# Kernel tuning notes

Hardware: AMD Instinct MI355X
Metric: run time of the kernel (lower is better)

## Reference

```python
import jax, jax.numpy as jnp
import numpy as np

B, S, E, H = 64, 100, 512, 1024  # H must equal 2*E (bmm in attention)
VS, VT, P = 32000, 32000, 100


def setup_inputs() -> dict:
    key = jax.random.key(0)
    ks = jax.random.split(key, 16)
    sc = 0.02
    return {
        "source_sentences": jax.random.randint(ks[0], (B, S), 0, VS),
        "positions": jax.random.randint(ks[1], (B, S), 0, P),
        "target_words": jax.random.randint(ks[2], (B,), 0, VT),
        "source_lengths": jnp.full((B,), S, dtype=jnp.int64 if jax.config.jax_enable_x64 else jnp.int32),
        "max_len": S,
        "emb_in": jax.random.normal(ks[3], (VS, E), jnp.float32) * sc,
        "emb_out": jax.random.normal(ks[4], (VT, E), jnp.float32) * sc,
        "emb_pos": jax.random.normal(ks[5], (P, E), jnp.float32) * sc,
        "W_scale": jax.random.normal(ks[6], (H, 2 * E), jnp.float32) * sc,
        "b_scale": jnp.zeros((H,), jnp.float32),
        "W_ih": jax.random.normal(ks[7], (H, E + H), jnp.float32) * sc,
        "b_ih": jnp.zeros((H,), jnp.float32),
        "W_hh": jax.random.normal(ks[8], (H, H), jnp.float32) * sc,
        "b_hh": jnp.zeros((H,), jnp.float32),
        "W_proj": jax.random.normal(ks[9], (VT, H), jnp.float32) * sc,
        "b_proj": jnp.zeros((VT,), jnp.float32),
    }


def reference(source_sentences, positions, target_words, source_lengths, max_len,
              emb_in, emb_out, emb_pos, W_scale, b_scale,
              W_ih, b_ih, W_hh, b_hh, W_proj, b_proj):
    # --- encoder_forward ---
    words = emb_in[source_sentences]              # [B,S,E]
    pos = emb_pos[positions]                      # [B,S,E]
    enc = jnp.concatenate([words, pos], axis=-1)  # [B,S,2E] combined embeddings
    h0 = jnp.mean(enc, axis=1) @ W_scale.T + b_scale  # [B,H]
    # --- attention (vectorized form of the per-position bmm loop) ---
    energy = jnp.einsum('bh,bsh->bs', h0, enc)        # [B,S]
    align = jax.nn.softmax(energy, axis=1)            # softmax over source positions
    # original uses torch.mean (not sum) over positions
    context = jnp.mean(align[:, :, None] * enc, axis=1)  # [B,2E] == [B,H]
    # --- decoder step ---
    out_w = emb_out[target_words]                      # [B,E]
    x = jnp.concatenate([out_w, context], axis=-1)     # [B,E+H]
    # nn.RNN single step, tanh nonlinearity
    h = jnp.tanh(x @ W_ih.T + b_ih + h0 @ W_hh.T + b_hh)  # [B,H]
    out = h @ W_proj.T + b_proj                        # [B,VT]
    return (out, h)
```

## Files before the change

kernel.cpp:

```cpp
#include <hip/hip_runtime.h>

typedef __attribute__((ext_vector_type(8))) __bf16 bf16x8;
typedef __attribute__((ext_vector_type(4))) float  f32x4;
typedef unsigned short u16;

__device__ __forceinline__ u16 f2bf(float f) {
    union { float f; unsigned int i; } v; v.f = f;
    unsigned int r = v.i + 0x7fffu + ((v.i >> 16) & 1u);
    return (u16)(r >> 16);
}
__device__ __forceinline__ unsigned pack2(float a, float b) {
    union { float f; unsigned u; } x, y; x.f = a; y.f = b;
    return __builtin_amdgcn_perm(y.u + 0x8000u, x.u + 0x8000u, 0x07060302u);
}

#define B_  64
#define S_  100
#define E_  512
#define H_  1024
#define VT_ 32000
#define Kc  128
#define PITCH 128
#define NS2 4
#define NS4 10


__global__ __launch_bounds__(256, 1)
void k1_encmean(const int* __restrict__ src, const int* __restrict__ pos,
                const float* __restrict__ emb_in, const float* __restrict__ emb_pos,
                u16* __restrict__ encmean) {
    int b = blockIdx.x, q4 = blockIdx.y, t = threadIdx.x;
    __shared__ int sidx[S_], pidx[S_];
    __shared__ float part[256][4];
    if (t < S_) { sidx[t] = src[b * S_ + t]; pidx[t] = pos[b * S_ + t]; }
    __syncthreads();

    int f4 = t & 63, g = t >> 6;
    bool isPos = (q4 >= 2);
    const float* base = isPos ? emb_pos : emb_in;
    const int*   idx  = isPos ? pidx : sidx;
    int col = (q4 & 1) * 256 + f4 * 4;

    float a0 = 0.f, a1 = 0.f, a2 = 0.f, a3 = 0.f;
    int s0 = g * 25;
    #pragma unroll
    for (int s = s0; s < s0 + 25; s++) {
        const float4 v = *(const float4*)(base + (size_t)idx[s] * E_ + col);
        a0 += v.x; a1 += v.y; a2 += v.z; a3 += v.w;
    }
    part[t][0] = a0; part[t][1] = a1; part[t][2] = a2; part[t][3] = a3;
    __syncthreads();

    if (t < 64) {
        const float inv = 1.0f / (float)S_;
        float r0 = 0.f, r1 = 0.f, r2 = 0.f, r3 = 0.f;
        #pragma unroll
        for (int g2 = 0; g2 < 4; g2++) {
            r0 += part[g2 * 64 + t][0]; r1 += part[g2 * 64 + t][1];
            r2 += part[g2 * 64 + t][2]; r3 += part[g2 * 64 + t][3];
        }
        int e = q4 * 256 + t * 4;
        u16* o = encmean + (size_t)b * (2 * E_) + e;
        o[0] = f2bf(r0 * inv); o[1] = f2bf(r1 * inv);
        o[2] = f2bf(r2 * inv); o[3] = f2bf(r3 * inv);
    }
}

#define MFMA16(a, bfrag, c) __builtin_amdgcn_mfma_f32_16x16x32_bf16((a), (bfrag), (c), 0, 0, 0)

template<int KLEN, int LDA, int LDW>
__device__ __forceinline__ void gemm_lds(const u16* __restrict__ A,
                                         const float* __restrict__ W,
                                         int jt, int koff, u16* __restrict__ ldsW,
                                         f32x4 acc[4], int t) {
    constexpr int NC = KLEN / Kc;
    const int lane = t & 63, w = t >> 6, m = lane & 15, q = lane >> 4;
    const int r = t >> 2, c4 = t & 3;
    const float* wsrc = W + (size_t)(jt + r) * LDW + koff + c4 * 4;
    const u16*   arow = A + (size_t)(w * 16 + m) * LDA + koff + q * 8;
    const int halfoff = (c4 & 1) * 4;

    float4 v[8];
    #pragma unroll
    for (int i = 0; i < 8; i++) v[i] = *(const float4*)(wsrc + i * 16);
    #pragma unroll
    for (int i = 0; i < 8; i++) {
        int U = (c4 >> 1) + 2 * i;
        uint2 p; p.x = pack2(v[i].x, v[i].y); p.y = pack2(v[i].z, v[i].w);
        *(uint2*)(ldsW + r * PITCH + ((U ^ (r & 15)) * 8) + halfoff) = p;
    }
    __syncthreads();

    for (int c = 0; c < NC; c++) {
        if (c + 1 < NC) {
            #pragma unroll
            for (int i = 0; i < 8; i++)
                v[i] = *(const float4*)(wsrc + (c + 1) * Kc + i * 16);
        }
        const u16* lb = ldsW + (c & 1) * (64 * PITCH);
        const u16* ar = arow + c * Kc;
        #pragma unroll
        for (int ks = 0; ks < 4; ks++) {
            bf16x8 a = *(const bf16x8*)(ar + ks * 32);
            #pragma unroll
            for (int f = 0; f < 4; f++) {
                int rr = f * 16 + m;
                int U  = ks * 4 + q;
                bf16x8 bfr = *(const bf16x8*)(lb + rr * PITCH + ((U ^ (rr & 15)) * 8));
                acc[f] = MFMA16(a, bfr, acc[f]);
            }
        }
        if (c + 1 < NC) {
            u16* wd = ldsW + ((c + 1) & 1) * (64 * PITCH) + r * PITCH;
            #pragma unroll
            for (int i = 0; i < 8; i++) {
                int U = (c4 >> 1) + 2 * i;
                uint2 p; p.x = pack2(v[i].x, v[i].y); p.y = pack2(v[i].z, v[i].w);
                *(uint2*)(wd + ((U ^ (r & 15)) * 8) + halfoff) = p;
            }
        }
        __syncthreads();
    }
}

__global__ __launch_bounds__(256, 2)
void k2_h0p(const u16* __restrict__ encmean, const float* __restrict__ Wscale,
            float* __restrict__ part2) {
    __shared__ u16 ldsW[2 * 64 * PITCH];
    int t = threadIdx.x, lane = t & 63, w = t >> 6, m = lane & 15, q = lane >> 4;
    int jt = blockIdx.x * 64, sp = blockIdx.y;
    f32x4 acc[4] = {{0,0,0,0},{0,0,0,0},{0,0,0,0},{0,0,0,0}};
    gemm_lds<256, 2 * E_, 2 * E_>(encmean, Wscale, jt, sp * 256, ldsW, acc, t);
    #pragma unroll
    for (int f = 0; f < 4; f++) {
        int j = jt + 16 * f + m;
        #pragma unroll
        for (int r2 = 0; r2 < 4; r2++) {
            int bb = w * 16 + q * 4 + r2;
            part2[(size_t)(sp * B_ + bb) * H_ + j] = acc[f][r2];
        }
    }
}

__global__ __launch_bounds__(256, 1)
void k3_attn(const int* __restrict__ src, const int* __restrict__ pos,
             const int* __restrict__ tgt,
             const float* __restrict__ emb_in, const float* __restrict__ emb_pos,
             const float* __restrict__ emb_out,
             const float* __restrict__ part2, const float* __restrict__ bscale,
             u16* __restrict__ x, u16* __restrict__ h0b) {
    int b = blockIdx.x, t = threadIdx.x;
    __shared__ float h0s[2 * E_];
    __shared__ int sidx[S_], pidx[S_];
    __shared__ float energy[S_];
    __shared__ float align_s[S_];

    for (int i = t; i < 2 * E_; i += 256) {
        float v = bscale[i];
        #pragma unroll
        for (int ks = 0; ks < NS2; ks++) v += part2[(size_t)(ks * B_ + b) * H_ + i];
        h0s[i] = v;
        h0b[(size_t)b * H_ + i] = f2bf(v);
    }
    if (t < S_) { sidx[t] = src[b * S_ + t]; pidx[t] = pos[b * S_ + t]; }
    __syncthreads();

    int lane = t & 63, w = t >> 6;
    for (int s = w; s < S_; s += 4) {
        const float* ri = emb_in  + (size_t)sidx[s] * E_;
        const float* rp = emb_pos + (size_t)pidx[s] * E_;
        float acc = 0.f;
        #pragma unroll
        for (int ii = 0; ii < 8; ii++) { int k = lane + 64 * ii; acc += ri[k] * h0s[k]; }
        #pragma unroll
        for (int ii = 0; ii < 8; ii++) { int k = lane + 64 * ii; acc += rp[k] * h0s[E_ + k]; }
        #pragma unroll
        for (int off = 32; off; off >>= 1) acc += __shfl_down(acc, off);
        if (lane == 0) energy[s] = acc;
    }
    __syncthreads();

    if (t < 64) {
        float e0 = energy[t];
        float e1 = (t + 64 < S_) ? energy[t + 64] : -1e30f;
        float mx = fmaxf(e0, e1);
        #pragma unroll
        for (int off = 32; off; off >>= 1) mx = fmaxf(mx, __shfl_xor(mx, off));
        float p0 = expf(e0 - mx);
        float p1 = (t + 64 < S_) ? expf(e1 - mx) : 0.f;
        float ss = p0 + p1;
        #pragma unroll
        for (int off = 32; off; off >>= 1) ss += __shfl_xor(ss, off);
        float inv = 1.0f / (ss * (float)S_);
        align_s[t] = p0 * inv;
        if (t + 64 < S_) align_s[t + 64] = p1 * inv;
    }
    __syncthreads();

    if (t < 128) {
        int o = t;
        bool isPos = (o >= 64);
        const float* base = isPos ? emb_pos : emb_in;
        const int* idx  = isPos ? pidx : sidx;
        int eo = (o & 63) * 8;
        float c[8] = {0,0,0,0,0,0,0,0};
        #pragma unroll 4
        for (int s = 0; s < S_; s++) {
            const float* row = base + (size_t)idx[s] * E_ + eo;
            float al = align_s[s];
            const float4 v0 = *(const float4*)(row);
            const float4 v1 = *(const float4*)(row + 4);
            c[0] += al * v0.x; c[1] += al * v0.y; c[2] += al * v0.z; c[3] += al * v0.w;
            c[4] += al * v1.x; c[5] += al * v1.y; c[6] += al * v1.z; c[7] += al * v1.w;
        }
        u16* xo = x + (size_t)b * (E_ + H_) + E_ + o * 8;
        #pragma unroll
        for (int i = 0; i < 8; i++) xo[i] = f2bf(c[i]);
    } else {
        int i = t - 128;
        int tw = tgt[b];
        const float4 v = *((const float4*)(emb_out + (size_t)tw * E_) + i);
        ushort4 o; o.x = f2bf(v.x); o.y = f2bf(v.y); o.z = f2bf(v.z); o.w = f2bf(v.w);
        *((ushort4*)(x + (size_t)b * (E_ + H_)) + i) = o;
    }
}

__global__ __launch_bounds__(256, 2)
void k4_hp(const u16* __restrict__ xb, const float* __restrict__ Wih,
           const u16* __restrict__ h0b, const float* __restrict__ Whh,
           float* __restrict__ part4) {
    __shared__ u16 ldsW[2 * 64 * PITCH];
    int t = threadIdx.x, lane = t & 63, w = t >> 6, m = lane & 15, q = lane >> 4;
    int jt = blockIdx.x * 64, sp = blockIdx.y;
    f32x4 acc[4] = {{0,0,0,0},{0,0,0,0},{0,0,0,0},{0,0,0,0}};
    if (sp < 6) gemm_lds<256, E_ + H_, E_ + H_>(xb,  Wih, jt, sp * 256,       ldsW, acc, t);
    else        gemm_lds<256, H_,      H_     >(h0b, Whh, jt, (sp - 6) * 256, ldsW, acc, t);
    #pragma unroll
    for (int f = 0; f < 4; f++) {
        int j = jt + 16 * f + m;
        #pragma unroll
        for (int r2 = 0; r2 < 4; r2++) {
            int bb = w * 16 + q * 4 + r2;
            part4[(size_t)(sp * B_ + bb) * H_ + j] = acc[f][r2];
        }
    }
}

__global__ __launch_bounds__(256, 1)
void k4_red(const float* __restrict__ part4,
            const float* __restrict__ bih, const float* __restrict__ bhh,
            float* __restrict__ houtf, u16* __restrict__ hbf) {
    int b = blockIdx.x, t = threadIdx.x;
    int j = t * 4;
    float4 s  = *(const float4*)(bih + j);
    const float4 b2 = *(const float4*)(bhh + j);
    s.x += b2.x; s.y += b2.y; s.z += b2.z; s.w += b2.w;
    #pragma unroll
    for (int ks = 0; ks < NS4; ks++) {
        const float4 p = *(const float4*)(part4 + (size_t)(ks * B_ + b) * H_ + j);
        s.x += p.x; s.y += p.y; s.z += p.z; s.w += p.w;
    }
    float4 h; h.x = tanhf(s.x); h.y = tanhf(s.y); h.z = tanhf(s.z); h.w = tanhf(s.w);
    *(float4*)(houtf + (size_t)b * H_ + j) = h;
    ushort4 o; o.x = f2bf(h.x); o.y = f2bf(h.y); o.z = f2bf(h.z); o.w = f2bf(h.w);
    *(ushort4*)(hbf + (size_t)b * H_ + j) = o;
}

__global__ __launch_bounds__(256, 2)
void k5_out(const u16* __restrict__ hb, const float* __restrict__ Wp,
            const float* __restrict__ bp, float* __restrict__ out) {
    __shared__ u16 ldsW[2 * 64 * PITCH];
    int t = threadIdx.x, lane = t & 63, w = t >> 6, m = lane & 15, q = lane >> 4;
    int jt = blockIdx.x * 64;
    f32x4 acc[4] = {{0,0,0,0},{0,0,0,0},{0,0,0,0},{0,0,0,0}};
    gemm_lds<H_, H_, H_>(hb, Wp, jt, 0, ldsW, acc, t);
    #pragma unroll
    for (int f = 0; f < 4; f++) {
        int j = jt + 16 * f + m;
        float bias = bp[j];
        #pragma unroll
        for (int r = 0; r < 4; r++) {
            int b = w * 16 + q * 4 + r;
            out[(size_t)b * VT_ + j] = acc[f][r] + bias;
        }
    }
}

extern "C" void kernel_launch(void* const* d_in, const int* in_sizes, int n_in,
                              void* d_out, int out_size, void* d_ws, size_t ws_size,
                              hipStream_t stream) {
    const int*   src     = (const int*)d_in[0];
    const int*   pos     = (const int*)d_in[1];
    const int*   tgt     = (const int*)d_in[2];
    const float* emb_in  = (const float*)d_in[5];
    const float* emb_out = (const float*)d_in[6];
    const float* emb_pos = (const float*)d_in[7];
    const float* Wscale  = (const float*)d_in[8];
    const float* bscale  = (const float*)d_in[9];
    const float* Wih     = (const float*)d_in[10];
    const float* bih     = (const float*)d_in[11];
    const float* Whh     = (const float*)d_in[12];
    const float* bhh     = (const float*)d_in[13];
    const float* Wproj   = (const float*)d_in[14];
    const float* bproj   = (const float*)d_in[15];

    char* ws = (char*)d_ws;
    u16*   encmean = (u16*)(ws);
    u16*   xb      = (u16*)(ws + 131072);
    u16*   h0b     = (u16*)(ws + 327680);
    u16*   hbf     = (u16*)(ws + 458752);
    float* part2   = (float*)(ws + 589824);
    float* part4   = (float*)(ws + 1638400);

    float* out   = (float*)d_out;
    float* houtf = out + (size_t)B_ * VT_;

    hipLaunchKernelGGL(k1_encmean, dim3(B_, 4),        dim3(256), 0, stream,
                       src, pos, emb_in, emb_pos, encmean);
    hipLaunchKernelGGL(k2_h0p,     dim3(H_ / 64, NS2), dim3(256), 0, stream,
                       encmean, Wscale, part2);
    hipLaunchKernelGGL(k3_attn,    dim3(B_),           dim3(256), 0, stream,
                       src, pos, tgt, emb_in, emb_pos, emb_out, part2, bscale,
                       xb, h0b);
    hipLaunchKernelGGL(k4_hp,      dim3(H_ / 64, NS4), dim3(256), 0, stream,
                       xb, Wih, h0b, Whh, part4);
    hipLaunchKernelGGL(k4_red,     dim3(B_),           dim3(256), 0, stream,
                       part4, bih, bhh, houtf, hbf);
    hipLaunchKernelGGL(k5_out,     dim3(VT_ / 64),     dim3(256), 0, stream,
                       hbf, Wproj, bproj, out);
}
```

Baseline: 319.6 us.

## Replace LDS-staged weight GEMM with direct register-loaded MFMA fragments; split attention context

Drops the LDS double-buffered weight staging in the GEMM helper. Each wave now loads its own fp32 weight rows from global memory, packs them to bf16 and feeds them straight into MFMA, looping over the four batch groups with A read from global. This removes the LDS stores and barriers on the weight-streaming path (the dominant cost is the 32000x1024 projection). The trade-off is less load coalescing and more global reads of the A operand. The attention kernel also splits the context reduction across all 256 threads via shared-memory partials, and launch bounds change for k2/k4.

```diff
diff --git a/kernel.cpp b/kernel.cpp
--- a/kernel.cpp
+++ b/kernel.cpp
@@ -19,8 +19,6 @@
 #define E_  512
 #define H_  1024
 #define VT_ 32000
-#define Kc  128
-#define PITCH 128
 #define NS2 4
 #define NS4 10
 
@@ -68,76 +66,43 @@
 
 #define MFMA16(a, bfrag, c) __builtin_amdgcn_mfma_f32_16x16x32_bf16((a), (bfrag), (c), 0, 0, 0)
 
-template<int KLEN, int LDA, int LDW>
-__device__ __forceinline__ void gemm_lds(const u16* __restrict__ A,
-                                         const float* __restrict__ W,
-                                         int jt, int koff, u16* __restrict__ ldsW,
-                                         f32x4 acc[4], int t) {
-    constexpr int NC = KLEN / Kc;
+template<int NKC, int LDA, int LDW>
+__device__ __forceinline__ void gemm_direct(const u16* __restrict__ A,
+                                            const float* __restrict__ W,
+                                            int jt, int koff, f32x4 acc[4], int t) {
     const int lane = t & 63, w = t >> 6, m = lane & 15, q = lane >> 4;
-    const int r = t >> 2, c4 = t & 3;
-    const float* wsrc = W + (size_t)(jt + r) * LDW + koff + c4 * 4;
-    const u16*   arow = A + (size_t)(w * 16 + m) * LDA + koff + q * 8;
-    const int halfoff = (c4 & 1) * 4;
-
-    float4 v[8];
-    #pragma unroll
-    for (int i = 0; i < 8; i++) v[i] = *(const float4*)(wsrc + i * 16);
-    #pragma unroll
-    for (int i = 0; i < 8; i++) {
-        int U = (c4 >> 1) + 2 * i;
-        uint2 p; p.x = pack2(v[i].x, v[i].y); p.y = pack2(v[i].z, v[i].w);
-        *(uint2*)(ldsW + r * PITCH + ((U ^ (r & 15)) * 8) + halfoff) = p;
-    }
-    __syncthreads();
-
-    for (int c = 0; c < NC; c++) {
-        if (c + 1 < NC) {
-            #pragma unroll
-            for (int i = 0; i < 8; i++)
-                v[i] = *(const float4*)(wsrc + (c + 1) * Kc + i * 16);
-        }
-        const u16* lb = ldsW + (c & 1) * (64 * PITCH);
-        const u16* ar = arow + c * Kc;
-        #pragma unroll
-        for (int ks = 0; ks < 4; ks++) {
-            bf16x8 a = *(const bf16x8*)(ar + ks * 32);
-            #pragma unroll
-            for (int f = 0; f < 4; f++) {
-                int rr = f * 16 + m;
-                int U  = ks * 4 + q;
-                bf16x8 bfr = *(const bf16x8*)(lb + rr * PITCH + ((U ^ (rr & 15)) * 8));
-                acc[f] = MFMA16(a, bfr, acc[f]);
-            }
-        }
-        if (c + 1 < NC) {
-            u16* wd = ldsW + ((c + 1) & 1) * (64 * PITCH) + r * PITCH;
-            #pragma unroll
-            for (int i = 0; i < 8; i++) {
-                int U = (c4 >> 1) + 2 * i;
-                uint2 p; p.x = pack2(v[i].x, v[i].y); p.y = pack2(v[i].z, v[i].w);
-                *(uint2*)(wd + ((U ^ (r & 15)) * 8) + halfoff) = p;
-            }
-        }
-        __syncthreads();
-    }
-}
-
-__global__ __launch_bounds__(256, 2)
+    const float* wrow = W + (size_t)(jt + w * 16 + m) * LDW + koff + q * 8;
+    const u16*   ab   = A + (size_t)m * LDA + koff + q * 8;
+    constexpr int UNR = (NKC <= 8) ? NKC : 4;
+    #pragma unroll UNR
+    for (int kk = 0; kk < NKC; kk++) {
+        const float4 w0 = *(const float4*)(wrow + kk * 32);
+        const float4 w1 = *(const float4*)(wrow + kk * 32 + 4);
+        union { unsigned u[4]; bf16x8 v; } bb;
+        bb.u[0] = pack2(w0.x, w0.y); bb.u[1] = pack2(w0.z, w0.w);
+        bb.u[2] = pack2(w1.x, w1.y); bb.u[3] = pack2(w1.z, w1.w);
+        #pragma unroll
+        for (int g = 0; g < 4; g++) {
+            bf16x8 a = *(const bf16x8*)(ab + (size_t)g * 16 * LDA + kk * 32);
+            acc[g] = MFMA16(a, bb.v, acc[g]);
+        }
+    }
+}
+
+__global__ __launch_bounds__(256, 1)
 void k2_h0p(const u16* __restrict__ encmean, const float* __restrict__ Wscale,
             float* __restrict__ part2) {
-    __shared__ u16 ldsW[2 * 64 * PITCH];
     int t = threadIdx.x, lane = t & 63, w = t >> 6, m = lane & 15, q = lane >> 4;
     int jt = blockIdx.x * 64, sp = blockIdx.y;
     f32x4 acc[4] = {{0,0,0,0},{0,0,0,0},{0,0,0,0},{0,0,0,0}};
-    gemm_lds<256, 2 * E_, 2 * E_>(encmean, Wscale, jt, sp * 256, ldsW, acc, t);
-    #pragma unroll
-    for (int f = 0; f < 4; f++) {
-        int j = jt + 16 * f + m;
+    gemm_direct<8, 2 * E_, 2 * E_>(encmean, Wscale, jt, sp * 256, acc, t);
+    int j = jt + w * 16 + m;
+    #pragma unroll
+    for (int g = 0; g < 4; g++) {
         #pragma unroll
         for (int r2 = 0; r2 < 4; r2++) {
-            int bb = w * 16 + q * 4 + r2;
-            part2[(size_t)(sp * B_ + bb) * H_ + j] = acc[f][r2];
+            int bb = g * 16 + q * 4 + r2;
+            part2[(size_t)(sp * B_ + bb) * H_ + j] = acc[g][r2];
         }
     }
 }
@@ -154,6 +119,7 @@
     __shared__ int sidx[S_], pidx[S_];
     __shared__ float energy[S_];
     __shared__ float align_s[S_];
+    __shared__ float cpart[128][8];
 
     for (int i = t; i < 2 * E_; i += 256) {
         float v = bscale[i];
@@ -166,6 +132,7 @@
     __syncthreads();
 
     int lane = t & 63, w = t >> 6;
+    #pragma unroll 5
     for (int s = w; s < S_; s += 4) {
         const float* ri = emb_in  + (size_t)sidx[s] * E_;
         const float* rp = emb_pos + (size_t)pidx[s] * E_;
@@ -197,15 +164,16 @@
     }
     __syncthreads();
 
-    if (t < 128) {
-        int o = t;
+    {
+        int g2 = t >> 7, o = t & 127;
         bool isPos = (o >= 64);
         const float* base = isPos ? emb_pos : emb_in;
         const int* idx  = isPos ? pidx : sidx;
         int eo = (o & 63) * 8;
         float c[8] = {0,0,0,0,0,0,0,0};
-        #pragma unroll 4
-        for (int s = 0; s < S_; s++) {
+        int s0 = g2 * 50;
+        #pragma unroll 5
+        for (int s = s0; s < s0 + 50; s++) {
             const float* row = base + (size_t)idx[s] * E_ + eo;
             float al = align_s[s];
             const float4 v0 = *(const float4*)(row);
@@ -213,35 +181,41 @@
             c[0] += al * v0.x; c[1] += al * v0.y; c[2] += al * v0.z; c[3] += al * v0.w;
             c[4] += al * v1.x; c[5] += al * v1.y; c[6] += al * v1.z; c[7] += al * v1.w;
         }
-        u16* xo = x + (size_t)b * (E_ + H_) + E_ + o * 8;
-        #pragma unroll
-        for (int i = 0; i < 8; i++) xo[i] = f2bf(c[i]);
-    } else {
-        int i = t - 128;
-        int tw = tgt[b];
-        const float4 v = *((const float4*)(emb_out + (size_t)tw * E_) + i);
-        ushort4 o; o.x = f2bf(v.x); o.y = f2bf(v.y); o.z = f2bf(v.z); o.w = f2bf(v.w);
-        *((ushort4*)(x + (size_t)b * (E_ + H_)) + i) = o;
-    }
-}
-
-__global__ __launch_bounds__(256, 2)
+        if (g2 == 1) {
+            #pragma unroll
+            for (int i = 0; i < 8; i++) cpart[o][i] = c[i];
+        }
+        __syncthreads();
+        if (g2 == 0) {
+            u16* xo = x + (size_t)b * (E_ + H_) + E_ + o * 8;
+            #pragma unroll
+            for (int i = 0; i < 8; i++) xo[i] = f2bf(c[i] + cpart[o][i]);
+        } else {
+            int tw = tgt[b];
+            const float4 v = *((const float4*)(emb_out + (size_t)tw * E_) + o);
+            ushort4 ov; ov.x = f2bf(v.x); ov.y = f2bf(v.y);
+            ov.z = f2bf(v.z); ov.w = f2bf(v.w);
+            *((ushort4*)(x + (size_t)b * (E_ + H_)) + o) = ov;
+        }
+    }
+}
+
+__global__ __launch_bounds__(256, 1)
 void k4_hp(const u16* __restrict__ xb, const float* __restrict__ Wih,
            const u16* __restrict__ h0b, const float* __restrict__ Whh,
            float* __restrict__ part4) {
-    __shared__ u16 ldsW[2 * 64 * PITCH];
     int t = threadIdx.x, lane = t & 63, w = t >> 6, m = lane & 15, q = lane >> 4;
     int jt = blockIdx.x * 64, sp = blockIdx.y;
     f32x4 acc[4] = {{0,0,0,0},{0,0,0,0},{0,0,0,0},{0,0,0,0}};
-    if (sp < 6) gemm_lds<256, E_ + H_, E_ + H_>(xb,  Wih, jt, sp * 256,       ldsW, acc, t);
-    else        gemm_lds<256, H_,      H_     >(h0b, Whh, jt, (sp - 6) * 256, ldsW, acc, t);
-    #pragma unroll
-    for (int f = 0; f < 4; f++) {
-        int j = jt + 16 * f + m;
+    if (sp < 6) gemm_direct<8, E_ + H_, E_ + H_>(xb,  Wih, jt, sp * 256,       acc, t);
+    else        gemm_direct<8, H_,      H_     >(h0b, Whh, jt, (sp - 6) * 256, acc, t);
+    int j = jt + w * 16 + m;
+    #pragma unroll
+    for (int g = 0; g < 4; g++) {
         #pragma unroll
         for (int r2 = 0; r2 < 4; r2++) {
-            int bb = w * 16 + q * 4 + r2;
-            part4[(size_t)(sp * B_ + bb) * H_ + j] = acc[f][r2];
+            int bb = g * 16 + q * 4 + r2;
+            part4[(size_t)(sp * B_ + bb) * H_ + j] = acc[g][r2];
         }
     }
 }
@@ -269,19 +243,18 @@
 __global__ __launch_bounds__(256, 2)
 void k5_out(const u16* __restrict__ hb, const float* __restrict__ Wp,
             const float* __restrict__ bp, float* __restrict__ out) {
-    __shared__ u16 ldsW[2 * 64 * PITCH];
     int t = threadIdx.x, lane = t & 63, w = t >> 6, m = lane & 15, q = lane >> 4;
     int jt = blockIdx.x * 64;
     f32x4 acc[4] = {{0,0,0,0},{0,0,0,0},{0,0,0,0},{0,0,0,0}};
-    gemm_lds<H_, H_, H_>(hb, Wp, jt, 0, ldsW, acc, t);
-    #pragma unroll
-    for (int f = 0; f < 4; f++) {
-        int j = jt + 16 * f + m;
-        float bias = bp[j];
+    gemm_direct<H_ / 32, H_, H_>(hb, Wp, jt, 0, acc, t);
+    int j = jt + w * 16 + m;
+    float bias = bp[j];
+    #pragma unroll
+    for (int g = 0; g < 4; g++) {
         #pragma unroll
         for (int r = 0; r < 4; r++) {
-            int b = w * 16 + q * 4 + r;
-            out[(size_t)b * VT_ + j] = acc[f][r] + bias;
+            int b = g * 16 + q * 4 + r;
+            out[(size_t)b * VT_ + j] = acc[g][r] + bias;
         }
     }
 }
```

After: 343.4 us. 7.5% more time.
